# Kernel tuning notes

Hardware: AMD Instinct MI355X
Metric: run time of the kernel (lower is better)

Reference implementation:

```python
import jax, jax.numpy as jnp
import numpy as np

N, E, EL = 50000, 150000, 300000   # atoms, bonds(=line-graph nodes), line-graph edges
FN, FE, FX = 128, 128, 64          # atom, bond, angle feature dims (encode_dim)
H, D = 4, 64                        # num_heads, per-head hidden
SLOPE = 0.01                        # torch leaky_relu default


def _leaky(x):
    return jnp.where(x >= 0, x, SLOPE * x)


def _seg_softmax(logits, seg, n):
    # softmax over edges grouped by destination (DGL edge_softmax). logits [E, H]
    m = jax.ops.segment_max(logits, seg, num_segments=n)
    ex = jnp.exp(logits - m[seg])
    s = jax.ops.segment_sum(ex, seg, num_segments=n)
    return ex / s[seg]


def _seg_mean(x, seg, n):
    # mean of incoming edge feats per dst node; empty segments -> 0 (DGL behavior)
    s = jax.ops.segment_sum(x, seg, num_segments=n)
    c = jax.ops.segment_sum(jnp.ones((x.shape[0], 1), x.dtype), seg, num_segments=n)
    return s / jnp.maximum(c, 1.0)


def setup_inputs() -> dict:
    key = jax.random.key(0)
    ks = iter(jax.random.split(key, 40))
    nrm = lambda shape, sc=0.1: jax.random.normal(next(ks), shape, jnp.float32) * sc
    z = lambda n: jnp.zeros((n,), jnp.float32)
    inp = {
        'nfeats': nrm((N, FN), 1.0),
        'efeats': nrm((E, FE), 1.0),
        'xfeats': nrm((EL, FX), 1.0),
        # EGAT layer (atom graph)
        'e_Wni': nrm((H * D, FN)), 'e_Wnj': nrm((H * D, FN)), 'e_Wfij': nrm((H * D, FE)),
        'e_Wnode': nrm((H * D, FN + FE)), 'e_bnode': z(H * D),
        'e_attn': nrm((H, D)), 'e_bias': z(H * D),
        # Path_Complex line-graph branch
        'lg_Wni': nrm((H * D, D)), 'lg_Wnj': nrm((H * D, D)), 'lg_Wfij': nrm((H * D, FX)),
        'lg_Wnode': nrm((H * D, D + FX)), 'lg_bnode': z(H * D),
        'lg_attn': nrm((H, D)), 'lg_bias': z(H * D),
        # Path_Complex graph branch
        'g_Wni': nrm((H * D, D)), 'g_Wnj': nrm((H * D, D)), 'g_Wfij': nrm((H * D, D)),
        'g_Wnode': nrm((H * D, D + D)), 'g_bnode': z(H * D),
        'g_attn': nrm((H, D)), 'g_bias': z(H * D),
        # graph / line-graph connectivity
        'src': jax.random.randint(next(ks), (E,), 0, N, jnp.int32),
        'dst': jax.random.randint(next(ks), (E,), 0, N, jnp.int32),
        'lsrc': jax.random.randint(next(ks), (EL,), 0, E, jnp.int32),
        'ldst': jax.random.randint(next(ks), (EL,), 0, E, jnp.int32),
    }
    return inp


def _forward(nfeats, efeats, xfeats,
             e_Wni, e_Wnj, e_Wfij, e_Wnode, e_bnode, e_attn, e_bias,
             lg_Wni, lg_Wnj, lg_Wfij, lg_Wnode, lg_bnode, lg_attn, lg_bias,
             g_Wni, g_Wnj, g_Wfij, g_Wnode, g_bnode, g_attn, g_bias,
             src, dst, lsrc, ldst):
    # ---- EGAT layer on atom graph ----
    fo = _leaky((nfeats @ e_Wni.T)[src] + (nfeats @ e_Wnj.T)[dst] + efeats @ e_Wfij.T + e_bias)
    fov = fo.reshape(E, H, D)
    e_att = _seg_softmax((fov * e_attn[None]).sum(-1), dst, N)      # [E, H]
    agg = _seg_mean(efeats, dst, N)                                   # [N, FE]
    h = (jnp.concatenate([nfeats, agg], 1) @ e_Wnode.T + e_bnode).reshape(N, H, D)
    h_node = _leaky(jax.ops.segment_sum(h[src] * e_att[:, :, None], dst, num_segments=N)).sum(1)
    f_edge = fov.sum(1)                                               # [E, D]

    # ---- Path_Complex layer: line-graph (bond->angle) branch ----
    lgf = _leaky((f_edge @ lg_Wni.T)[lsrc] + (f_edge @ lg_Wnj.T)[ldst] + xfeats @ lg_Wfij.T + lg_bias)
    lgv = lgf.reshape(EL, H, D)
    a_lg = _seg_softmax((lgv * lg_attn[None]).sum(-1), ldst, E)      # [EL, H]
    aggx = _seg_mean(xfeats, ldst, E)                                 # [E, FX]
    m1 = (jnp.concatenate([f_edge, aggx], 1) @ lg_Wnode.T + lg_bnode).reshape(E, H, D)
    lg_h = _leaky(jax.ops.segment_sum(m1[lsrc] * a_lg[:, :, None], ldst, num_segments=E)).sum(1)

    # ---- Path_Complex layer: graph (atom->bond) branch ----
    gf = _leaky((h_node @ g_Wni.T)[src] + (h_node @ g_Wnj.T)[dst] + f_edge @ g_Wfij.T + g_bias)
    gv = gf.reshape(E, H, D)
    a_g = _seg_softmax((gv * g_attn[None]).sum(-1), dst, N)          # [E, H] -> l_graph ndata 'a'
    node_edge = h_node[src] + h_node[dst]
    m2 = (jnp.concatenate([node_edge, f_edge], 1) @ g_Wnode.T + g_bnode).reshape(E, H, D)
    # u_mul_v on line graph: message = h_out[lsrc] * a[ldst]
    g_h = _leaky(jax.ops.segment_sum(m2[lsrc] * a_g[ldst][:, :, None], ldst, num_segments=E)).sum(1)

    return g_h + lg_h                                                 # [E, D] updated bond feats


def reference(nfeats, efeats, xfeats,
              e_Wni, e_Wnj, e_Wfij, e_Wnode, e_bnode, e_attn, e_bias,
              lg_Wni, lg_Wnj, lg_Wfij, lg_Wnode, lg_bnode, lg_attn, lg_bias,
              g_Wni, g_Wnj, g_Wfij, g_Wnode, g_bnode, g_attn, g_bias,
              src, dst, lsrc, ldst):
    return _forward(nfeats, efeats, xfeats,
                    e_Wni, e_Wnj, e_Wfij, e_Wnode, e_bnode, e_attn, e_bias,
                    lg_Wni, lg_Wnj, lg_Wfij, lg_Wnode, lg_bnode, lg_attn, lg_bias,
                    g_Wni, g_Wnj, g_Wfij, g_Wnode, g_bnode, g_attn, g_bias,
                    src, dst, lsrc, ldst)
```

## Files before the change

### kernel.cpp

```cpp
#include <hip/hip_runtime.h>
#include <hip/hip_bf16.h>
#include <math.h>

typedef __hip_bfloat16 bf16;
typedef short bf16x8 __attribute__((ext_vector_type(8)));
typedef short s16x4 __attribute__((ext_vector_type(4)));
typedef float f32x4 __attribute__((ext_vector_type(4)));

__device__ __forceinline__ float b2f(bf16 x) { return __bfloat162float(x); }
__device__ __forceinline__ bf16  f2b(float x) { return __float2bfloat16(x); }
__device__ __forceinline__ float leaky(float x) { return x >= 0.0f ? x : 0.01f * x; }
__device__ __forceinline__ float sb2f(short s) {
  return __uint_as_float(((unsigned)(unsigned short)s) << 16);
}
__device__ __forceinline__ short f2bs(float x) {
  unsigned u = __float_as_uint(x);
  u += 0x7FFFu + ((u >> 16) & 1u);
  return (short)(u >> 16);
}
__device__ __forceinline__ float ldF(const void* p, size_t i, int f) {
  return f ? ((const float*)p)[i] : b2f(((const bf16*)p)[i]);
}
__device__ __forceinline__ bf16x8 ldA8(const char* row, int k, int f) {
  if (!f) return *(const bf16x8*)(row + (size_t)k * 2);
  const float4* p = (const float4*)(row + (size_t)k * 4);
  float4 a = p[0], b = p[1];
  bf16x8 r;
  r[0] = f2bs(a.x); r[1] = f2bs(a.y); r[2] = f2bs(a.z); r[3] = f2bs(a.w);
  r[4] = f2bs(b.x); r[5] = f2bs(b.y); r[6] = f2bs(b.z); r[7] = f2bs(b.w);
  return r;
}
__device__ __forceinline__ bf16x8 ldA8sum(const bf16* base, int K0, int s, int t, int k) {
  bf16x8 u = *(const bf16x8*)(base + (size_t)s * K0 + k);
  bf16x8 v = *(const bf16x8*)(base + (size_t)t * K0 + k);
  bf16x8 r;
#pragma unroll
  for (int j = 0; j < 8; ++j) r[j] = f2bs(sb2f(u[j]) + sb2f(v[j]));
  return r;
}

__global__ void k_detect(const unsigned* __restrict__ w, int* __restrict__ flag) {
  __shared__ int cnt[256];
  unsigned x = w[threadIdx.x];
  unsigned ex = (x >> 7) & 0xFFu;
  cnt[threadIdx.x] = (ex >= 96u && ex <= 144u) ? 1 : 0;
  __syncthreads();
  for (int s = 128; s > 0; s >>= 1) {
    if (threadIdx.x < s) cnt[threadIdx.x] += cnt[threadIdx.x + s];
    __syncthreads();
  }
  if (threadIdx.x == 0) *flag = (cnt[0] < 128) ? 1 : 0;
}

struct WArgs { const void* src[21]; int beg[22]; int len[21]; };
__global__ void k_cvt_all(WArgs wa, bf16* __restrict__ dst, int total,
                          const int* __restrict__ flagp) {
  int f = *flagp;
  for (int i = blockIdx.x * 256 + threadIdx.x; i < total; i += gridDim.x * 256) {
    int t = 0;
    while (t < 20 && i >= wa.beg[t + 1]) ++t;
    int loc = i - wa.beg[t];
    bf16 v = f2b(0.0f);
    if (loc < wa.len[t])
      v = f ? f2b(((const float*)wa.src[t])[loc]) : ((const bf16*)wa.src[t])[loc];
    dst[i] = v;
  }
}

__global__ void k_cvt3(const float* __restrict__ a, bf16* __restrict__ da, size_t na,
                       const float* __restrict__ b, bf16* __restrict__ db, size_t nb,
                       const float* __restrict__ c, bf16* __restrict__ dc, size_t nc,
                       const int* __restrict__ flagp) {
  if (!*flagp) return;
  size_t tot = (na + nb + nc) >> 2;
  for (size_t i = (size_t)blockIdx.x * 256 + threadIdx.x; i < tot;
       i += (size_t)gridDim.x * 256) {
    size_t j = i << 2;
    const float* s; bf16* d; size_t loc;
    if (j < na)           { s = a; d = da; loc = j; }
    else if (j < na + nb) { s = b; d = db; loc = j - na; }
    else                  { s = c; d = dc; loc = j - na - nb; }
    float4 v = *(const float4*)(s + loc);
    s16x4 o; o[0] = f2bs(v.x); o[1] = f2bs(v.y); o[2] = f2bs(v.z); o[3] = f2bs(v.w);
    *(s16x4*)(d + loc) = o;
  }
}

__global__ void k_izero(int* __restrict__ p, int n) {
  int i = blockIdx.x * 256 + threadIdx.x;
  for (; i < n; i += gridDim.x * 256) p[i] = 0;
}

__global__ void k_hist(const int* __restrict__ seg, int* __restrict__ deg, int n) {
  int i = blockIdx.x * 256 + threadIdx.x;
  if (i < n) atomicAdd(&deg[seg[i]], 1);
}

__global__ __launch_bounds__(256)
void k_scan_local(const int* __restrict__ deg, int* __restrict__ rp,
                  int* __restrict__ bsum, int n) {
  __shared__ int sh[256];
  int tid = threadIdx.x;
  int base = blockIdx.x * 4096 + tid * 16;
  int v[16]; int s = 0;
#pragma unroll
  for (int j = 0; j < 16; ++j) { v[j] = (base + j < n) ? deg[base + j] : 0; s += v[j]; }
  sh[tid] = s;
  __syncthreads();
  for (int o = 1; o < 256; o <<= 1) {
    int t = (tid >= o) ? sh[tid - o] : 0;
    __syncthreads();
    sh[tid] += t;
    __syncthreads();
  }
  int run = sh[tid] - s;
#pragma unroll
  for (int j = 0; j < 16; ++j) {
    run += v[j];
    if (base + j < n) rp[base + j + 1] = run;
  }
  if (tid == 255) bsum[blockIdx.x] = sh[255];
  if (blockIdx.x == 0 && tid == 0) rp[0] = 0;
}
__global__ __launch_bounds__(256)
void k_scan_bsum(int* __restrict__ bsum, int nb) {
  __shared__ int sh[256];
  __shared__ int carry;
  int tid = threadIdx.x;
  if (tid == 0) carry = 0;
  __syncthreads();
  for (int base = 0; base < nb; base += 256) {
    int i = base + tid;
    int v = (i < nb) ? bsum[i] : 0;
    sh[tid] = v;
    __syncthreads();
    for (int o = 1; o < 256; o <<= 1) {
      int t = (tid >= o) ? sh[tid - o] : 0;
      __syncthreads();
      sh[tid] += t;
      __syncthreads();
    }
    if (i < nb) bsum[i] = carry + sh[tid] - v;
    int tot = sh[255];
    __syncthreads();
    if (tid == 0) carry += tot;
    __syncthreads();
  }
}
__global__ __launch_bounds__(256)
void k_scan_add(int* __restrict__ rp, const int* __restrict__ bsum, int n) {
  int b = blockIdx.x + 1;
  int ofs = bsum[b];
  int base = b * 4096 + threadIdx.x * 16;
#pragma unroll
  for (int j = 0; j < 16; ++j) {
    int idx = base + j + 1;
    if (idx <= n) rp[idx] += ofs;
  }
}

__global__ void k_slot(const int* __restrict__ seg, const int* __restrict__ rp,
                       int* __restrict__ cur, int* __restrict__ eid,
                       const int* __restrict__ aux, int* __restrict__ auxval,
                       int* __restrict__ pos, int n) {
  int i = blockIdx.x * 256 + threadIdx.x;
  if (i >= n) return;
  int t = seg[i];
  int p = atomicAdd(&cur[t], 1);
  int j = rp[t] + p;
  eid[j] = i;
  if (auxval) auxval[j] = aux[i];
  if (pos) pos[i] = j;
}

__global__ void k_gmean(const void* __restrict__ X, const void* __restrict__ Xc, int mode,
                        const int* __restrict__ rp, const int* __restrict__ eid,
                        bf16* __restrict__ out, int n, int width,
                        const int* __restrict__ flagp) {
  int f = (mode == 2) ? *flagp : mode;
  if (Xc && f) { X = Xc; f = 0; }
  int d = threadIdx.x;
  int row = blockIdx.x * blockDim.y + threadIdx.y;
  if (row >= n) return;
  int b = rp[row], e = rp[row + 1];
  float s = 0.0f;
  for (int j = b; j < e; ++j) s += ldF(X, (size_t)eid[j] * width + d, f);
  out[(size_t)row * width + d] = f2b(s / fmaxf((float)(e - b), 1.0f));
}

__global__ __launch_bounds__(256)
void k_mgemm(const void* __restrict__ A0, const void* __restrict__ A0c, int m0mode, int K0,
             const void* __restrict__ A1, int m1mode, int Ktot,
             const bf16* __restrict__ W, int whs, const bf16* __restrict__ bias,
             bf16* __restrict__ C, int cs, int M,
             const int* __restrict__ gs, const int* __restrict__ gd,
             const int* __restrict__ flagp) {
  int tid = threadIdx.x;
  int w = tid >> 6, lane = tid & 63, l15 = lane & 15, q = lane >> 4;
  int h = blockIdx.y;
  int fl = *flagp;
  int f0 = (m0mode == 2) ? fl : m0mode;
  if (A0c && f0) { A0 = A0c; f0 = 0; }
  int f1 = (m1mode == 2) ? fl : m1mode;
  const bf16* Wh = W + (size_t)h * whs;
  int colofs = h * 64;
  int m0 = blockIdx.x * 64 + w * 16;
  int mA = m0 + l15; if (mA > M - 1) mA = M - 1;
  int sA = 0, tA = 0;
  const char* rowA0 = nullptr;
  if (gs) { sA = gs[mA]; tA = gd[mA]; }
  else rowA0 = (const char*)A0 + (size_t)mA * K0 * (f0 ? 4 : 2);
  const char* rowA1 = A1 ? (const char*)A1 + (size_t)mA * (Ktot - K0) * (f1 ? 4 : 2) : nullptr;

  f32x4 acc[4] = {{0,0,0,0},{0,0,0,0},{0,0,0,0},{0,0,0,0}};
  for (int k = q * 8; k < Ktot; k += 32) {
    bf16x8 a;
    if (k < K0) a = gs ? ldA8sum((const bf16*)A0, K0, sA, tA, k) : ldA8(rowA0, k, f0);
    else        a = ldA8(rowA1, k - K0, f1);
    const bf16* wb = Wh + (size_t)l15 * Ktot + k;
#pragma unroll
    for (int t = 0; t < 4; ++t)
      acc[t] = __builtin_amdgcn_mfma_f32_16x16x32_bf16(
          a, *(const bf16x8*)(wb + (size_t)(t * 16) * Ktot), acc[t], 0, 0, 0);
  }
#pragma unroll
  for (int t = 0; t < 4; ++t) {
    int col = t * 16 + l15;
    float bv = bias ? b2f(bias[colofs + col]) : 0.0f;
#pragma unroll
    for (int r = 0; r < 4; ++r) {
      int m = m0 + q * 4 + r;
      if (m < M) C[(size_t)m * cs + colofs + col] = f2b(acc[t][r] + bv);
    }
  }
}

__global__ __launch_bounds__(256)
void k_mgemm2(const void* __restrict__ A, const void* __restrict__ Ac, int mode, int K,
              const bf16* __restrict__ W1, const bf16* __restrict__ W2, int whs,
              bf16* __restrict__ C1, bf16* __restrict__ C2, int cs, int M,
              const int* __restrict__ flagp) {
  int tid = threadIdx.x;
  int w = tid >> 6, lane = tid & 63, l15 = lane & 15, q = lane >> 4;
  int h = blockIdx.y;
  int f = (mode == 2) ? *flagp : mode;
  if (Ac && f) { A = Ac; f = 0; }
  const bf16* W1h = W1 + (size_t)h * whs;
  const bf16* W2h = W2 + (size_t)h * whs;
  int colofs = h * 64;
  int m0 = blockIdx.x * 64 + w * 16;
  int mA = m0 + l15; if (mA > M - 1) mA = M - 1;
  const char* rowA = (const char*)A + (size_t)mA * K * (f ? 4 : 2);

  f32x4 a1[4] = {{0,0,0,0},{0,0,0,0},{0,0,0,0},{0,0,0,0}};
  f32x4 a2[4] = {{0,0,0,0},{0,0,0,0},{0,0,0,0},{0,0,0,0}};
  for (int k = q * 8; k < K; k += 32) {
    bf16x8 a = ldA8(rowA, k, f);
    const bf16* w1 = W1h + (size_t)l15 * K + k;
    const bf16* w2 = W2h + (size_t)l15 * K + k;
#pragma unroll
    for (int t = 0; t < 4; ++t) {
      a1[t] = __builtin_amdgcn_mfma_f32_16x16x32_bf16(
          a, *(const bf16x8*)(w1 + (size_t)(t * 16) * K), a1[t], 0, 0, 0);
      a2[t] = __builtin_amdgcn_mfma_f32_16x16x32_bf16(
          a, *(const bf16x8*)(w2 + (size_t)(t * 16) * K), a2[t], 0, 0, 0);
    }
  }
#pragma unroll
  for (int r = 0; r < 4; ++r) {
    int m = m0 + q * 4 + r;
    if (m < M) {
      s16x4 o1, o2;
#pragma unroll
      for (int t = 0; t < 4; ++t) { o1[t] = f2bs(a1[t][r]); o2[t] = f2bs(a2[t][r]); }
      *(s16x4*)(C1 + (size_t)m * cs + colofs + l15 * 4) = o1;
      *(s16x4*)(C2 + (size_t)m * cs + colofs + l15 * 4) = o2;
    }
  }
}

template<int NK>
__global__ __launch_bounds__(256)
void k_mcomb4(const void* __restrict__ A, const void* __restrict__ Ac, int mode,
              const bf16* __restrict__ W, int whs,
              const bf16* __restrict__ bias, const bf16* __restrict__ attn,
              const bf16* __restrict__ G1, const bf16* __restrict__ G2, int gstr,
              const int* __restrict__ gi, const int* __restrict__ gj,
              const int* __restrict__ posw,
              float* __restrict__ lg4, bf16* __restrict__ fout,
              int M, const int* __restrict__ flagp) {
  constexpr int K = NK * 32;
  int tid = threadIdx.x;
  int w = tid >> 6, lane = tid & 63, l15 = lane & 15, q = lane >> 4;
  int f = (mode == 2) ? *flagp : mode;
  if (Ac && f) { A = Ac; f = 0; }
  int m0 = blockIdx.x * 64 + w * 16;
  int mA = m0 + l15; if (mA > M - 1) mA = M - 1;
  const char* rowA = (const char*)A + (size_t)mA * K * (f ? 4 : 2);
  bf16x8 af[NK];
#pragma unroll
  for (int i = 0; i < NK; ++i) af[i] = ldA8(rowA, q * 8 + 32 * i, f);
  int sIdx[4], dIdx[4], pIdx[4]; bool okr[4];
#pragma unroll
  for (int r = 0; r < 4; ++r) {
    int m = m0 + q * 4 + r;
    okr[r] = m < M; int mc = okr[r] ? m : M - 1;
    sIdx[r] = gi[mc]; dIdx[r] = gj[mc];
    pIdx[r] = posw ? posw[mc] : mc;
  }
  s16x4 gv1[4][4], gv2[4][4];
#pragma unroll
  for (int r = 0; r < 4; ++r) {
    const s16x4* p1 = (const s16x4*)(G1 + (size_t)sIdx[r] * gstr) + l15;
    const s16x4* p2 = (const s16x4*)(G2 + (size_t)dIdx[r] * gstr) + l15;
#pragma unroll
    for (int h = 0; h < 4; ++h) { gv1[r][h] = p1[h * 16]; gv2[r][h] = p2[h * 16]; }
  }
  f32x4 fs[4] = {{0,0,0,0},{0,0,0,0},{0,0,0,0},{0,0,0,0}};
#pragma unroll
  for (int h = 0; h < 4; ++h) {
    const bf16* Wh = W + (size_t)h * whs;
    f32x4 acc[4] = {{0,0,0,0},{0,0,0,0},{0,0,0,0},{0,0,0,0}};
#pragma unroll
    for (int i = 0; i < NK; ++i) {
      const bf16* wb = Wh + (size_t)l15 * K + q * 8 + 32 * i;
#pragma unroll
      for (int t = 0; t < 4; ++t)
        acc[t] = __builtin_amdgcn_mfma_f32_16x16x32_bf16(
            af[i], *(const bf16x8*)(wb + (size_t)(t * 16) * K), acc[t], 0, 0, 0);
    }
    float bv[4], av[4];
#pragma unroll
    for (int t = 0; t < 4; ++t) {
      bv[t] = b2f(bias[h * 64 + t * 16 + l15]);
      av[t] = b2f(attn[h * 64 + t * 16 + l15]);
    }
    float part[4];
#pragma unroll
    for (int r = 0; r < 4; ++r) {
      float p = 0.0f;
#pragma unroll
      for (int t = 0; t < 4; ++t) {
        float v = acc[t][r] + bv[t] + sb2f(gv1[r][h][t]) + sb2f(gv2[r][h][t]);
        v = leaky(v);
        p += v * av[t];
        fs[t][r] += v;
      }
      part[r] = p;
    }
#pragma unroll
    for (int o = 1; o < 16; o <<= 1)
#pragma unroll
      for (int r = 0; r < 4; ++r) part[r] += __shfl_xor(part[r], o, 64);
    if (l15 == 0) {
#pragma unroll
      for (int r = 0; r < 4; ++r)
        if (okr[r]) lg4[(size_t)pIdx[r] * 4 + h] = part[r];
    }
  }
  if (fout) {
#pragma unroll
    for (int t = 0; t < 4; ++t) {
      int col = t * 16 + l15;
#pragma unroll
      for (int r = 0; r < 4; ++r)
        if (okr[r]) fout[(size_t)(m0 + q * 4 + r) * 64 + col] = f2b(fs[t][r]);
    }
  }
}

__global__ __launch_bounds__(256)
void k_mcomb(const void* __restrict__ A, const void* __restrict__ Ac, int mode, int K,
             const bf16* __restrict__ W, const bf16* __restrict__ bias,
             const bf16* __restrict__ attn,
             const bf16* __restrict__ G1, const bf16* __restrict__ G2, int gstr,
             const int* __restrict__ gi, const int* __restrict__ gj,
             const int* __restrict__ posw,
             float* __restrict__ lg, int M, const int* __restrict__ flagp) {
  int tid = threadIdx.x;
  int w = tid >> 6, lane = tid & 63, l15 = lane & 15, q = lane >> 4;
  int f = (mode == 2) ? *flagp : mode;
  if (Ac && f) { A = Ac; f = 0; }
  int m0 = blockIdx.x * 64 + w * 16;
  int mA = m0 + l15; if (mA > M - 1) mA = M - 1;
  const char* rowA = (const char*)A + (size_t)mA * K * (f ? 4 : 2);
  int mcs[4], pIdx[4]; bool okr[4];
#pragma unroll
  for (int r = 0; r < 4; ++r) {
    int m = m0 + q * 4 + r;
    okr[r] = m < M; mcs[r] = okr[r] ? m : M - 1;
    pIdx[r] = posw ? posw[mcs[r]] : mcs[r];
  }
  s16x4 gv1[4], gv2[4];
#pragma unroll
  for (int r = 0; r < 4; ++r) {
    gv1[r] = ((const s16x4*)(G1 + (size_t)gi[mcs[r]] * gstr))[l15];
    gv2[r] = ((const s16x4*)(G2 + (size_t)gj[mcs[r]] * gstr))[l15];
  }
  f32x4 acc[4] = {{0,0,0,0},{0,0,0,0},{0,0,0,0},{0,0,0,0}};
  for (int k = q * 8; k < K; k += 32) {
    bf16x8 a = ldA8(rowA, k, f);
    const bf16* wb = W + (size_t)l15 * K + k;
#pragma unroll
    for (int t = 0; t < 4; ++t)
      acc[t] = __builtin_amdgcn_mfma_f32_16x16x32_bf16(
          a, *(const bf16x8*)(wb + (size_t)(t * 16) * K), acc[t], 0, 0, 0);
  }
  float attv[4], bsv[4];
#pragma unroll
  for (int t = 0; t < 4; ++t) { attv[t] = b2f(attn[t*16+l15]); bsv[t] = b2f(bias[t*16+l15]); }
  float part[4];
#pragma unroll
  for (int r = 0; r < 4; ++r) {
    float p = 0.0f;
#pragma unroll
    for (int t = 0; t < 4; ++t) {
      float v = acc[t][r] + bsv[t] + sb2f(gv1[r][t]) + sb2f(gv2[r][t]);
      p += leaky(v) * attv[t];
    }
    part[r] = p;
  }
#pragma unroll
  for (int o = 1; o < 16; o <<= 1)
#pragma unroll
    for (int r = 0; r < 4; ++r) part[r] += __shfl_xor(part[r], o, 64);
  if (l15 == 0) {
#pragma unroll
    for (int r = 0; r < 4; ++r)
      if (okr[r]) lg[pIdx[r]] = part[r];
  }
}

__global__ __launch_bounds__(256)
void k_smax4_csr(float* __restrict__ lg, const int* __restrict__ rp, int n) {
  int tid = blockIdx.x * 256 + threadIdx.x;
  int row = tid >> 2, h = tid & 3;
  if (row >= n) return;
  int b = rp[row], e = rp[row + 1];
  float m = -INFINITY;
  for (int j = b; j < e; ++j) m = fmaxf(m, lg[(size_t)j * 4 + h]);
  float s = 0.0f;
  for (int j = b; j < e; ++j) {
    float ex = expf(lg[(size_t)j * 4 + h] - m);
    lg[(size_t)j * 4 + h] = ex;
    s += ex;
  }
  float inv = 1.0f / s;
  for (int j = b; j < e; ++j) lg[(size_t)j * 4 + h] *= inv;
}
__global__ __launch_bounds__(256)
void k_smax4_eid(float* __restrict__ lg, const int* __restrict__ rp,
                 const int* __restrict__ eid, int n) {
  int tid = blockIdx.x * 256 + threadIdx.x;
  int row = tid >> 2, h = tid & 3;
  if (row >= n) return;
  int b = rp[row], e = rp[row + 1];
  float m = -INFINITY;
  for (int j = b; j < e; ++j) m = fmaxf(m, lg[(size_t)eid[j] * 4 + h]);
  float s = 0.0f;
  for (int j = b; j < e; ++j) {
    float ex = expf(lg[(size_t)eid[j] * 4 + h] - m);
    lg[(size_t)eid[j] * 4 + h] = ex;
    s += ex;
  }
  float inv = 1.0f / s;
  for (int j = b; j < e; ++j) lg[(size_t)eid[j] * 4 + h] *= inv;
}
__global__ __launch_bounds__(256)
void k_smax1_csr(float* __restrict__ lg, const int* __restrict__ rp, int n) {
  int row = blockIdx.x * 256 + threadIdx.x;
  if (row >= n) return;
  int b = rp[row], e = rp[row + 1];
  float m = -INFINITY;
  for (int j = b; j < e; ++j) m = fmaxf(m, lg[j]);
  float s = 0.0f;
  for (int j = b; j < e; ++j) { float ex = expf(lg[j] - m); lg[j] = ex; s += ex; }
  float inv = 1.0f / s;
  for (int j = b; j < e; ++j) lg[j] *= inv;
}

__global__ __launch_bounds__(256)
void k_ghnode(const bf16* __restrict__ H, const float* __restrict__ lg4c,
              const int* __restrict__ rp, const int* __restrict__ srcv,
              bf16* __restrict__ hnode, int N) {
  int d = threadIdx.x, h = threadIdx.y;
  int n = blockIdx.x;
  int b = rp[n], e = rp[n + 1];
  float s = 0.0f;
  for (int j = b; j < e; ++j)
    s += b2f(H[(size_t)srcv[j] * 256 + h * 64 + d]) * lg4c[(size_t)j * 4 + h];
  float v = leaky(s);
  __shared__ float sh[4][64];
  if (h > 0) sh[h][d] = v;
  __syncthreads();
  if (h == 0)
    hnode[(size_t)n * 64 + d] = f2b(v + sh[1][d] + sh[2][d] + sh[3][d]);
}

__global__ void k_gout2(const bf16* __restrict__ M1, const float* __restrict__ lgE,
                        const int* __restrict__ rp, const int* __restrict__ lsv,
                        float* __restrict__ out, int E, int first) {
  int d = threadIdx.x;
  int t = blockIdx.x * 4 + threadIdx.y;
  if (t >= E) return;
  int b = rp[t], e = rp[t + 1];
  float s = 0.0f;
  for (int j = b; j < e; ++j)
    s += b2f(M1[(size_t)lsv[j] * 64 + d]) * lgE[j];
  float val = leaky(s);
  if (first) out[(size_t)t * 64 + d] = val;
  else       out[(size_t)t * 64 + d] += val;
}

__global__ void k_gout3(const bf16* __restrict__ M2, const float* __restrict__ lg4n,
                        const int* __restrict__ rp, const int* __restrict__ lsv,
                        float* __restrict__ out, int E, int h) {
  int d = threadIdx.x;
  int t = blockIdx.x * 4 + threadIdx.y;
  if (t >= E) return;
  int b = rp[t], e = rp[t + 1];
  float s = 0.0f;
  for (int j = b; j < e; ++j) s += b2f(M2[(size_t)lsv[j] * 64 + d]);
  float a = lg4n[(size_t)t * 4 + h];
  out[(size_t)t * 64 + d] += leaky(a * s);
}

__global__ void k_addpair(const bf16* __restrict__ hn, const int* __restrict__ src,
                          const int* __restrict__ dst, bf16* __restrict__ ne, int E) {
  int d = threadIdx.x;
  int e = blockIdx.x * 4 + threadIdx.y;
  if (e >= E) return;
  ne[(size_t)e * 64 + d] =
      f2b(b2f(hn[(size_t)src[e] * 64 + d]) + b2f(hn[(size_t)dst[e] * 64 + d]));
}

__global__ void k_cast(void* __restrict__ out, const float* __restrict__ a, size_t n,
                       const int* __restrict__ flagp) {
  int f = *flagp;
  size_t i = (size_t)blockIdx.x * blockDim.x + threadIdx.x;
  size_t st = (size_t)gridDim.x * blockDim.x;
  for (; i < n; i += st) {
    if (f) ((float*)out)[i] = a[i];
    else   ((bf16*)out)[i] = f2b(a[i]);
  }
}

extern "C" void kernel_launch(void* const* d_in, const int* in_sizes, int n_in,
                              void* d_out, int out_size, void* d_ws, size_t ws_size,
                              hipStream_t stream) {
  const int* src  = (const int*)d_in[24];
  const int* dst  = (const int*)d_in[25];
  const int* lsrc = (const int*)d_in[26];
  const int* ldst = (const int*)d_in[27];

  const int N  = in_sizes[0] / 128;
  const int E  = in_sizes[24];
  const int EL = in_sizes[26];
  (void)n_in; (void)out_size; (void)ws_size;

  char* base = (char*)d_ws;
  size_t off = 0;
  auto alloc = [&](size_t bytes) -> char* {
    char* p = base + off;
    off = (off + bytes + 255) & ~(size_t)255;
    return p;
  };
  int* flag = (int*)alloc(256);
  size_t wofs[28]; size_t wtot = 0;
  for (int i = 3; i <= 23; ++i) { wofs[i] = wtot; wtot += (size_t)((in_sizes[i] + 127) & ~127); }
  bf16* WA = (bf16*)alloc(wtot * 2);

  int*   tmpi  = (int*)alloc((size_t)2 * E * 4);
  int*   rpN   = (int*)alloc((size_t)(N + 1) * 4);
  int*   eidN  = (int*)alloc((size_t)E * 4);
  int*   srcv  = (int*)alloc((size_t)E * 4);
  int*   posN  = (int*)alloc((size_t)E * 4);
  int*   rpE   = (int*)alloc((size_t)(E + 1) * 4);
  int*   eidEL = (int*)alloc((size_t)EL * 4);
  int*   lsv   = (int*)alloc((size_t)EL * 4);
  int*   posE  = (int*)alloc((size_t)EL * 4);
  int*   bsum  = (int*)alloc(((size_t)((E > N ? E : N) + 4095) / 4096 + 8) * 4);
  bf16*  fedge = (bf16*)alloc((size_t)E * 64 * 2);
  bf16*  hnode = (bf16*)alloc((size_t)N * 64 * 2);
  float* outacc= (float*)alloc((size_t)E * 64 * 4);
  bf16*  aggB  = (bf16*)alloc((size_t)E * 64 * 2);
  bf16*  SA    = (bf16*)alloc((size_t)N * 256 * 2 > (size_t)E * 64 * 2
                              ? (size_t)N * 256 * 2 : (size_t)E * 64 * 2);
  bf16*  SB    = (bf16*)alloc((size_t)N * 256 * 2 > (size_t)E * 64 * 2
                              ? (size_t)N * 256 * 2 : (size_t)E * 64 * 2);
  float* logE4 = (float*)alloc((size_t)E * 4 * 4);
  float* logh  = (float*)alloc((size_t)EL * 4);
  bf16*  nb    = (bf16*)alloc((size_t)N * 128 * 2);

  bf16* eb = (bf16*)outacc;
  bf16* xb = (bf16*)d_out;

  dim3 blk(256);
  const unsigned tN = (N + 63) / 64, tEg = (E + 63) / 64, tELg = (EL + 63) / 64;
  const unsigned gE4 = (E + 3) / 4, gN4 = (N + 3) / 4;
  const unsigned cE = (E + 255) / 256, cEL = (EL + 255) / 256;
  const int nbN = (N + 4095) / 4096, nbE = (E + 4095) / 4096;

  k_detect<<<dim3(1), blk, 0, stream>>>((const unsigned*)d_in[0], flag);
  WArgs wa;
  for (int i = 3; i <= 23; ++i) {
    wa.src[i - 3] = d_in[i];
    wa.beg[i - 3] = (int)wofs[i];
    wa.len[i - 3] = in_sizes[i];
  }
  wa.beg[21] = (int)wtot;
  k_cvt_all<<<dim3(512), blk, 0, stream>>>(wa, WA, (int)wtot, flag);
  k_cvt3<<<dim3(2048), blk, 0, stream>>>(
      (const float*)d_in[0], nb, (size_t)N * 128,
      (const float*)d_in[1], eb, (size_t)E * 128,
      (const float*)d_in[2], xb, (size_t)EL * 64, flag);

  int* deg = tmpi; int* cur = tmpi + E;
  k_izero<<<dim3(1024), blk, 0, stream>>>(tmpi, 2 * E);
  k_hist<<<dim3(cE), blk, 0, stream>>>(dst, deg, E);
  k_scan_local<<<dim3(nbN), blk, 0, stream>>>(deg, rpN, bsum, N);
  k_scan_bsum<<<dim3(1), blk, 0, stream>>>(bsum, nbN);
  if (nbN > 1) k_scan_add<<<dim3(nbN - 1), blk, 0, stream>>>(rpN, bsum, N);
  k_slot<<<dim3(cE), blk, 0, stream>>>(dst, rpN, cur, eidN, src, srcv, posN, E);
  k_izero<<<dim3(1024), blk, 0, stream>>>(tmpi, 2 * E);
  k_hist<<<dim3(cEL), blk, 0, stream>>>(ldst, deg, EL);
  k_scan_local<<<dim3(nbE), blk, 0, stream>>>(deg, rpE, bsum, E);
  k_scan_bsum<<<dim3(1), blk, 0, stream>>>(bsum, nbE);
  if (nbE > 1) k_scan_add<<<dim3(nbE - 1), blk, 0, stream>>>(rpE, bsum, E);
  k_slot<<<dim3(cEL), blk, 0, stream>>>(ldst, rpE, cur, eidEL, lsrc, lsv, posE, EL);

  k_gmean<<<dim3((N + 1) / 2), dim3(128, 2), 0, stream>>>(d_in[1], eb, 2, rpN, eidN,
                                                          aggB, N, 128, flag);
  k_mgemm2<<<dim3(tN, 4), blk, 0, stream>>>(d_in[0], nb, 2, 128, WA + wofs[3], WA + wofs[4],
                                            8192, SA, SB, 256, N, flag);
  k_mcomb4<4><<<dim3(tEg), blk, 0, stream>>>(d_in[1], eb, 2, WA + wofs[5], 8192,
      WA + wofs[9], WA + wofs[8], SA, SB, 256, src, dst, posN, logE4, fedge, E, flag);
  k_smax4_csr<<<dim3((N * 4 + 255) / 256), blk, 0, stream>>>(logE4, rpN, N);
  k_mgemm<<<dim3(tN, 4), blk, 0, stream>>>(d_in[0], nb, 2, 128, aggB, 0, 256,
      WA + wofs[6], 16384, WA + wofs[7], SA, 256, N, nullptr, nullptr, flag);
  k_ghnode<<<dim3(N), dim3(64, 4), 0, stream>>>(SA, logE4, rpN, srcv, hnode, N);

  k_gmean<<<dim3(gE4), dim3(64, 4), 0, stream>>>(d_in[2], xb, 2, rpE, eidEL, aggB, E, 64, flag);
  for (int h = 0; h < 4; ++h) {
    k_mgemm2<<<dim3(tEg), blk, 0, stream>>>(fedge, nullptr, 0, 64,
        WA + wofs[10] + h * 4096, WA + wofs[11] + h * 4096, 0, SA, SB, 64, E, flag);
    k_mcomb<<<dim3(tELg), blk, 0, stream>>>(d_in[2], xb, 2, 64,
        WA + wofs[12] + h * 4096, WA + wofs[16] + h * 64, WA + wofs[15] + h * 64,
        SA, SB, 64, lsrc, ldst, posE, logh, EL, flag);
    k_smax1_csr<<<dim3((E + 255) / 256), blk, 0, stream>>>(logh, rpE, E);
    k_mgemm<<<dim3(tEg, 1), blk, 0, stream>>>(fedge, nullptr, 0, 64, aggB, 0, 128,
        WA + wofs[13] + (size_t)h * 8192, 0, WA + wofs[14] + h * 64,
        SA, 64, E, nullptr, nullptr, flag);
    k_gout2<<<dim3(gE4), dim3(64, 4), 0, stream>>>(SA, logh, rpE, lsv,
                                                   outacc, E, h == 0 ? 1 : 0);
  }

  k_mgemm2<<<dim3(tN, 4), blk, 0, stream>>>(hnode, nullptr, 0, 64, WA + wofs[17], WA + wofs[18],
                                            4096, SA, SB, 256, N, flag);
  k_mcomb4<2><<<dim3(tEg), blk, 0, stream>>>(fedge, nullptr, 0, WA + wofs[19], 4096,
      WA + wofs[23], WA + wofs[22], SA, SB, 256, src, dst, nullptr, logE4, nullptr, E, flag);
  k_smax4_eid<<<dim3((N * 4 + 255) / 256), blk, 0, stream>>>(logE4, rpN, eidN, N);
  k_addpair<<<dim3(gE4), dim3(64, 4), 0, stream>>>(hnode, src, dst, aggB, E);
  for (int h = 0; h < 4; ++h) {
    k_mgemm<<<dim3(tEg, 1), blk, 0, stream>>>(aggB, nullptr, 0, 64, fedge, 0, 128,
        WA + wofs[20] + (size_t)h * 8192, 0, WA + wofs[21] + h * 64,
        SB, 64, E, nullptr, nullptr, flag);
    k_gout3<<<dim3(gE4), dim3(64, 4), 0, stream>>>(SB, logE4, rpE, lsv,
                                                   outacc, E, h);
  }

  k_cast<<<dim3(2048), blk, 0, stream>>>(d_out, outacc, (size_t)E * 64, flag);
}
```

Measured before the change: 1.804 ms.

## Permute bond data into dst-sorted CSR order and translate indices accordingly

Bond features and all bond-indexed intermediates (fedge, logE4, aggregated messages) are now stored in dst-sorted CSR order. A gather kernel builds the permuted bf16 copy, and line-graph indices are remapped through posN. This lets the atom-level mean and softmax read contiguous rows instead of going through eid indirection, and it removes the separate eid-based softmax kernel. In exchange it adds a permutation pass, an index translation kernel and extra index arrays, and the final outputs must be mapped back through posN lookups.

```diff
diff --git a/kernel.cpp b/kernel.cpp
--- a/kernel.cpp
+++ b/kernel.cpp
@@ -67,22 +67,38 @@
   }
 }
 
-__global__ void k_cvt3(const float* __restrict__ a, bf16* __restrict__ da, size_t na,
-                       const float* __restrict__ b, bf16* __restrict__ db, size_t nb,
+__global__ void k_cvt2(const float* __restrict__ a, bf16* __restrict__ da, size_t na,
                        const float* __restrict__ c, bf16* __restrict__ dc, size_t nc,
                        const int* __restrict__ flagp) {
   if (!*flagp) return;
-  size_t tot = (na + nb + nc) >> 2;
+  size_t tot = (na + nc) >> 2;
   for (size_t i = (size_t)blockIdx.x * 256 + threadIdx.x; i < tot;
        i += (size_t)gridDim.x * 256) {
     size_t j = i << 2;
     const float* s; bf16* d; size_t loc;
-    if (j < na)           { s = a; d = da; loc = j; }
-    else if (j < na + nb) { s = b; d = db; loc = j - na; }
-    else                  { s = c; d = dc; loc = j - na - nb; }
+    if (j < na) { s = a; d = da; loc = j; }
+    else        { s = c; d = dc; loc = j - na; }
     float4 v = *(const float4*)(s + loc);
     s16x4 o; o[0] = f2bs(v.x); o[1] = f2bs(v.y); o[2] = f2bs(v.z); o[3] = f2bs(v.w);
     *(s16x4*)(d + loc) = o;
+  }
+}
+
+__global__ void k_cvtp(const void* __restrict__ X, const int* __restrict__ eid,
+                       bf16* __restrict__ out, int n, const int* __restrict__ flagp) {
+  int f = *flagp;
+  int row = blockIdx.x * 4 + threadIdx.y;
+  if (row >= n) return;
+  int e = eid[row];
+  int d0 = threadIdx.x * 2;
+  if (f) {
+    float2 v = *(const float2*)((const float*)X + (size_t)e * 128 + d0);
+    unsigned pack = ((unsigned)(unsigned short)f2bs(v.y) << 16) |
+                    (unsigned)(unsigned short)f2bs(v.x);
+    *(unsigned*)((char*)out + (size_t)row * 256 + d0 * 2) = pack;
+  } else {
+    *(unsigned*)((char*)out + (size_t)row * 256 + d0 * 2) =
+        *(const unsigned*)((const char*)X + (size_t)e * 256 + d0 * 2);
   }
 }
 
@@ -161,7 +177,8 @@
 
 __global__ void k_slot(const int* __restrict__ seg, const int* __restrict__ rp,
                        int* __restrict__ cur, int* __restrict__ eid,
-                       const int* __restrict__ aux, int* __restrict__ auxval,
+                       const int* __restrict__ aux1, int* __restrict__ av1,
+                       const int* __restrict__ aux2, int* __restrict__ av2,
                        int* __restrict__ pos, int n) {
   int i = blockIdx.x * 256 + threadIdx.x;
   if (i >= n) return;
@@ -169,12 +186,25 @@
   int p = atomicAdd(&cur[t], 1);
   int j = rp[t] + p;
   eid[j] = i;
-  if (auxval) auxval[j] = aux[i];
+  if (av1) av1[j] = aux1[i];
+  if (av2) av2[j] = aux2[i];
   if (pos) pos[i] = j;
+}
+
+__global__ void k_xlat(const int* __restrict__ lsrc, const int* __restrict__ ldst,
+                       const int* __restrict__ posN,
+                       int* __restrict__ lsvE, int* __restrict__ ldvE,
+                       int* __restrict__ lsvC, int n) {
+  int i = blockIdx.x * 256 + threadIdx.x;
+  if (i >= n) return;
+  lsvE[i] = posN[lsrc[i]];
+  ldvE[i] = posN[ldst[i]];
+  lsvC[i] = posN[lsvC[i]];
 }
 
 __global__ void k_gmean(const void* __restrict__ X, const void* __restrict__ Xc, int mode,
                         const int* __restrict__ rp, const int* __restrict__ eid,
+                        const int* __restrict__ orow,
                         bf16* __restrict__ out, int n, int width,
                         const int* __restrict__ flagp) {
   int f = (mode == 2) ? *flagp : mode;
@@ -184,8 +214,10 @@
   if (row >= n) return;
   int b = rp[row], e = rp[row + 1];
   float s = 0.0f;
-  for (int j = b; j < e; ++j) s += ldF(X, (size_t)eid[j] * width + d, f);
-  out[(size_t)row * width + d] = f2b(s / fmaxf((float)(e - b), 1.0f));
+  for (int j = b; j < e; ++j)
+    s += ldF(X, (size_t)(eid ? eid[j] : j) * width + d, f);
+  int orw = orow ? orow[row] : row;
+  out[(size_t)orw * width + d] = f2b(s / fmaxf((float)(e - b), 1.0f));
 }
 
 __global__ __launch_bounds__(256)
@@ -193,7 +225,6 @@
              const void* __restrict__ A1, int m1mode, int Ktot,
              const bf16* __restrict__ W, int whs, const bf16* __restrict__ bias,
              bf16* __restrict__ C, int cs, int M,
-             const int* __restrict__ gs, const int* __restrict__ gd,
              const int* __restrict__ flagp) {
   int tid = threadIdx.x;
   int w = tid >> 6, lane = tid & 63, l15 = lane & 15, q = lane >> 4;
@@ -206,16 +237,13 @@
   int colofs = h * 64;
   int m0 = blockIdx.x * 64 + w * 16;
   int mA = m0 + l15; if (mA > M - 1) mA = M - 1;
-  int sA = 0, tA = 0;
-  const char* rowA0 = nullptr;
-  if (gs) { sA = gs[mA]; tA = gd[mA]; }
-  else rowA0 = (const char*)A0 + (size_t)mA * K0 * (f0 ? 4 : 2);
+  const char* rowA0 = (const char*)A0 + (size_t)mA * K0 * (f0 ? 4 : 2);
   const char* rowA1 = A1 ? (const char*)A1 + (size_t)mA * (Ktot - K0) * (f1 ? 4 : 2) : nullptr;
 
   f32x4 acc[4] = {{0,0,0,0},{0,0,0,0},{0,0,0,0},{0,0,0,0}};
   for (int k = q * 8; k < Ktot; k += 32) {
     bf16x8 a;
-    if (k < K0) a = gs ? ldA8sum((const bf16*)A0, K0, sA, tA, k) : ldA8(rowA0, k, f0);
+    if (k < K0) a = ldA8(rowA0, k, f0);
     else        a = ldA8(rowA1, k - K0, f1);
     const bf16* wb = Wh + (size_t)l15 * Ktot + k;
 #pragma unroll
@@ -281,32 +309,28 @@
 
 template<int NK>
 __global__ __launch_bounds__(256)
-void k_mcomb4(const void* __restrict__ A, const void* __restrict__ Ac, int mode,
-              const bf16* __restrict__ W, int whs,
-              const bf16* __restrict__ bias, const bf16* __restrict__ attn,
-              const bf16* __restrict__ G1, const bf16* __restrict__ G2, int gstr,
-              const int* __restrict__ gi, const int* __restrict__ gj,
-              const int* __restrict__ posw,
-              float* __restrict__ lg4, bf16* __restrict__ fout,
-              int M, const int* __restrict__ flagp) {
+void k_mcomb4C(const bf16* __restrict__ A,
+               const bf16* __restrict__ W, int whs,
+               const bf16* __restrict__ bias, const bf16* __restrict__ attn,
+               const bf16* __restrict__ G1, const bf16* __restrict__ G2, int gstr,
+               const int* __restrict__ sv, const int* __restrict__ dv,
+               float* __restrict__ lg4, bf16* __restrict__ fout, int M) {
   constexpr int K = NK * 32;
   int tid = threadIdx.x;
   int w = tid >> 6, lane = tid & 63, l15 = lane & 15, q = lane >> 4;
-  int f = (mode == 2) ? *flagp : mode;
-  if (Ac && f) { A = Ac; f = 0; }
   int m0 = blockIdx.x * 64 + w * 16;
   int mA = m0 + l15; if (mA > M - 1) mA = M - 1;
-  const char* rowA = (const char*)A + (size_t)mA * K * (f ? 4 : 2);
+  const bf16* rowA = A + (size_t)mA * K;
   bf16x8 af[NK];
 #pragma unroll
-  for (int i = 0; i < NK; ++i) af[i] = ldA8(rowA, q * 8 + 32 * i, f);
-  int sIdx[4], dIdx[4], pIdx[4]; bool okr[4];
+  for (int i = 0; i < NK; ++i) af[i] = *(const bf16x8*)(rowA + q * 8 + 32 * i);
+  int sIdx[4], dIdx[4], mcs[4]; bool okr[4];
 #pragma unroll
   for (int r = 0; r < 4; ++r) {
     int m = m0 + q * 4 + r;
     okr[r] = m < M; int mc = okr[r] ? m : M - 1;
-    sIdx[r] = gi[mc]; dIdx[r] = gj[mc];
-    pIdx[r] = posw ? posw[mc] : mc;
+    mcs[r] = mc;
+    sIdx[r] = sv[mc]; dIdx[r] = dv[mc];
   }
   s16x4 gv1[4][4], gv2[4][4];
 #pragma unroll
@@ -355,7 +379,7 @@
     if (l15 == 0) {
 #pragma unroll
       for (int r = 0; r < 4; ++r)
-        if (okr[r]) lg4[(size_t)pIdx[r] * 4 + h] = part[r];
+        if (okr[r]) lg4[(size_t)mcs[r] * 4 + h] = part[r];
     }
   }
   if (fout) {
@@ -449,24 +473,6 @@
   for (int j = b; j < e; ++j) lg[(size_t)j * 4 + h] *= inv;
 }
 __global__ __launch_bounds__(256)
-void k_smax4_eid(float* __restrict__ lg, const int* __restrict__ rp,
-                 const int* __restrict__ eid, int n) {
-  int tid = blockIdx.x * 256 + threadIdx.x;
-  int row = tid >> 2, h = tid & 3;
-  if (row >= n) return;
-  int b = rp[row], e = rp[row + 1];
-  float m = -INFINITY;
-  for (int j = b; j < e; ++j) m = fmaxf(m, lg[(size_t)eid[j] * 4 + h]);
-  float s = 0.0f;
-  for (int j = b; j < e; ++j) {
-    float ex = expf(lg[(size_t)eid[j] * 4 + h] - m);
-    lg[(size_t)eid[j] * 4 + h] = ex;
-    s += ex;
-  }
-  float inv = 1.0f / s;
-  for (int j = b; j < e; ++j) lg[(size_t)eid[j] * 4 + h] *= inv;
-}
-__global__ __launch_bounds__(256)
 void k_smax1_csr(float* __restrict__ lg, const int* __restrict__ rp, int n) {
   int row = blockIdx.x * 256 + threadIdx.x;
   if (row >= n) return;
@@ -513,6 +519,7 @@
 }
 
 __global__ void k_gout3(const bf16* __restrict__ M2, const float* __restrict__ lg4n,
+                        const int* __restrict__ posN,
                         const int* __restrict__ rp, const int* __restrict__ lsv,
                         float* __restrict__ out, int E, int h) {
   int d = threadIdx.x;
@@ -521,17 +528,17 @@
   int b = rp[t], e = rp[t + 1];
   float s = 0.0f;
   for (int j = b; j < e; ++j) s += b2f(M2[(size_t)lsv[j] * 64 + d]);
-  float a = lg4n[(size_t)t * 4 + h];
+  float a = lg4n[(size_t)posN[t] * 4 + h];
   out[(size_t)t * 64 + d] += leaky(a * s);
 }
 
-__global__ void k_addpair(const bf16* __restrict__ hn, const int* __restrict__ src,
-                          const int* __restrict__ dst, bf16* __restrict__ ne, int E) {
+__global__ void k_addpairC(const bf16* __restrict__ hn, const int* __restrict__ sv,
+                           const int* __restrict__ dv, bf16* __restrict__ ne, int E) {
   int d = threadIdx.x;
-  int e = blockIdx.x * 4 + threadIdx.y;
-  if (e >= E) return;
-  ne[(size_t)e * 64 + d] =
-      f2b(b2f(hn[(size_t)src[e] * 64 + d]) + b2f(hn[(size_t)dst[e] * 64 + d]));
+  int j = blockIdx.x * 4 + threadIdx.y;
+  if (j >= E) return;
+  ne[(size_t)j * 64 + d] =
+      f2b(b2f(hn[(size_t)sv[j] * 64 + d]) + b2f(hn[(size_t)dv[j] * 64 + d]));
 }
 
 __global__ void k_cast(void* __restrict__ out, const float* __restrict__ a, size_t n,
@@ -574,10 +581,13 @@
   int*   rpN   = (int*)alloc((size_t)(N + 1) * 4);
   int*   eidN  = (int*)alloc((size_t)E * 4);
   int*   srcv  = (int*)alloc((size_t)E * 4);
+  int*   dstv  = (int*)alloc((size_t)E * 4);
   int*   posN  = (int*)alloc((size_t)E * 4);
   int*   rpE   = (int*)alloc((size_t)(E + 1) * 4);
   int*   eidEL = (int*)alloc((size_t)EL * 4);
   int*   lsv   = (int*)alloc((size_t)EL * 4);
+  int*   lsvE  = (int*)alloc((size_t)EL * 4);
+  int*   ldvE  = (int*)alloc((size_t)EL * 4);
   int*   posE  = (int*)alloc((size_t)EL * 4);
   int*   bsum  = (int*)alloc(((size_t)((E > N ? E : N) + 4095) / 4096 + 8) * 4);
   bf16*  fedge = (bf16*)alloc((size_t)E * 64 * 2);
@@ -592,12 +602,12 @@
   float* logh  = (float*)alloc((size_t)EL * 4);
   bf16*  nb    = (bf16*)alloc((size_t)N * 128 * 2);
 
-  bf16* eb = (bf16*)outacc;
-  bf16* xb = (bf16*)d_out;
+  bf16* ebC = (bf16*)outacc;
+  bf16* xb  = (bf16*)d_out;
 
   dim3 blk(256);
   const unsigned tN = (N + 63) / 64, tEg = (E + 63) / 64, tELg = (EL + 63) / 64;
-  const unsigned gE4 = (E + 3) / 4, gN4 = (N + 3) / 4;
+  const unsigned gE4 = (E + 3) / 4;
   const unsigned cE = (E + 255) / 256, cEL = (EL + 255) / 256;
   const int nbN = (N + 4095) / 4096, nbE = (E + 4095) / 4096;
 
@@ -610,9 +620,8 @@
   }
   wa.beg[21] = (int)wtot;
   k_cvt_all<<<dim3(512), blk, 0, stream>>>(wa, WA, (int)wtot, flag);
-  k_cvt3<<<dim3(2048), blk, 0, stream>>>(
+  k_cvt2<<<dim3(2048), blk, 0, stream>>>(
       (const float*)d_in[0], nb, (size_t)N * 128,
-      (const float*)d_in[1], eb, (size_t)E * 128,
       (const float*)d_in[2], xb, (size_t)EL * 64, flag);
 
   int* deg = tmpi; int* cur = tmpi + E;
@@ -621,51 +630,55 @@
   k_scan_local<<<dim3(nbN), blk, 0, stream>>>(deg, rpN, bsum, N);
   k_scan_bsum<<<dim3(1), blk, 0, stream>>>(bsum, nbN);
   if (nbN > 1) k_scan_add<<<dim3(nbN - 1), blk, 0, stream>>>(rpN, bsum, N);
-  k_slot<<<dim3(cE), blk, 0, stream>>>(dst, rpN, cur, eidN, src, srcv, posN, E);
+  k_slot<<<dim3(cE), blk, 0, stream>>>(dst, rpN, cur, eidN, src, srcv, dst, dstv, posN, E);
+  k_cvtp<<<dim3(gE4), dim3(64, 4), 0, stream>>>(d_in[1], eidN, ebC, E, flag);
   k_izero<<<dim3(1024), blk, 0, stream>>>(tmpi, 2 * E);
   k_hist<<<dim3(cEL), blk, 0, stream>>>(ldst, deg, EL);
   k_scan_local<<<dim3(nbE), blk, 0, stream>>>(deg, rpE, bsum, E);
   k_scan_bsum<<<dim3(1), blk, 0, stream>>>(bsum, nbE);
   if (nbE > 1) k_scan_add<<<dim3(nbE - 1), blk, 0, stream>>>(rpE, bsum, E);
-  k_slot<<<dim3(cEL), blk, 0, stream>>>(ldst, rpE, cur, eidEL, lsrc, lsv, posE, EL);
-
-  k_gmean<<<dim3((N + 1) / 2), dim3(128, 2), 0, stream>>>(d_in[1], eb, 2, rpN, eidN,
-                                                          aggB, N, 128, flag);
+  k_slot<<<dim3(cEL), blk, 0, stream>>>(ldst, rpE, cur, eidEL, lsrc, lsv, nullptr, nullptr,
+                                        posE, EL);
+  k_xlat<<<dim3(cEL), blk, 0, stream>>>(lsrc, ldst, posN, lsvE, ldvE, lsv, EL);
+
+  k_gmean<<<dim3((N + 1) / 2), dim3(128, 2), 0, stream>>>(ebC, nullptr, 0, rpN, nullptr,
+                                                          nullptr, aggB, N, 128, flag);
   k_mgemm2<<<dim3(tN, 4), blk, 0, stream>>>(d_in[0], nb, 2, 128, WA + wofs[3], WA + wofs[4],
                                             8192, SA, SB, 256, N, flag);
-  k_mcomb4<4><<<dim3(tEg), blk, 0, stream>>>(d_in[1], eb, 2, WA + wofs[5], 8192,
-      WA + wofs[9], WA + wofs[8], SA, SB, 256, src, dst, posN, logE4, fedge, E, flag);
+  k_mcomb4C<4><<<dim3(tEg), blk, 0, stream>>>(ebC, WA + wofs[5], 8192,
+      WA + wofs[9], WA + wofs[8], SA, SB, 256, srcv, dstv, logE4, fedge, E);
   k_smax4_csr<<<dim3((N * 4 + 255) / 256), blk, 0, stream>>>(logE4, rpN, N);
   k_mgemm<<<dim3(tN, 4), blk, 0, stream>>>(d_in[0], nb, 2, 128, aggB, 0, 256,
-      WA + wofs[6], 16384, WA + wofs[7], SA, 256, N, nullptr, nullptr, flag);
+      WA + wofs[6], 16384, WA + wofs[7], SA, 256, N, flag);
   k_ghnode<<<dim3(N), dim3(64, 4), 0, stream>>>(SA, logE4, rpN, srcv, hnode, N);
 
-  k_gmean<<<dim3(gE4), dim3(64, 4), 0, stream>>>(d_in[2], xb, 2, rpE, eidEL, aggB, E, 64, flag);
+  k_gmean<<<dim3(gE4), dim3(64, 4), 0, stream>>>(d_in[2], xb, 2, rpE, eidEL, posN,
+                                                 aggB, E, 64, flag);
   for (int h = 0; h < 4; ++h) {
     k_mgemm2<<<dim3(tEg), blk, 0, stream>>>(fedge, nullptr, 0, 64,
         WA + wofs[10] + h * 4096, WA + wofs[11] + h * 4096, 0, SA, SB, 64, E, flag);
     k_mcomb<<<dim3(tELg), blk, 0, stream>>>(d_in[2], xb, 2, 64,
         WA + wofs[12] + h * 4096, WA + wofs[16] + h * 64, WA + wofs[15] + h * 64,
-        SA, SB, 64, lsrc, ldst, posE, logh, EL, flag);
+        SA, SB, 64, lsvE, ldvE, posE, logh, EL, flag);
     k_smax1_csr<<<dim3((E + 255) / 256), blk, 0, stream>>>(logh, rpE, E);
     k_mgemm<<<dim3(tEg, 1), blk, 0, stream>>>(fedge, nullptr, 0, 64, aggB, 0, 128,
         WA + wofs[13] + (size_t)h * 8192, 0, WA + wofs[14] + h * 64,
-        SA, 64, E, nullptr, nullptr, flag);
+        SA, 64, E, flag);
     k_gout2<<<dim3(gE4), dim3(64, 4), 0, stream>>>(SA, logh, rpE, lsv,
                                                    outacc, E, h == 0 ? 1 : 0);
   }
 
-  k_mgemm2<<<dim3(tN, 4), blk, 0, stream>>>(hnode, nullptr, 0, 64, WA + wofs[17], WA + wofs[18],
-                                            4096, SA, SB, 256, N, flag);
-  k_mcomb4<2><<<dim3(tEg), blk, 0, stream>>>(fedge, nullptr, 0, WA + wofs[19], 4096,
-      WA + wofs[23], WA + wofs[22], SA, SB, 256, src, dst, nullptr, logE4, nullptr, E, flag);
-  k_smax4_eid<<<dim3((N * 4 + 255) / 256), blk, 0, stream>>>(logE4, rpN, eidN, N);
-  k_addpair<<<dim3(gE4), dim3(64, 4), 0, stream>>>(hnode, src, dst, aggB, E);
+  k_mgemm2<<<dim3(tN, 4), blk, 0, stream>>>(hnode, nullptr, 0, 64, WA + wofs[17],
+                                            WA + wofs[18], 4096, SA, SB, 256, N, flag);
+  k_mcomb4C<2><<<dim3(tEg), blk, 0, stream>>>(fedge, WA + wofs[19], 4096,
+      WA + wofs[23], WA + wofs[22], SA, SB, 256, srcv, dstv, logE4, nullptr, E);
+  k_smax4_csr<<<dim3((N * 4 + 255) / 256), blk, 0, stream>>>(logE4, rpN, N);
+  k_addpairC<<<dim3(gE4), dim3(64, 4), 0, stream>>>(hnode, srcv, dstv, aggB, E);
   for (int h = 0; h < 4; ++h) {
     k_mgemm<<<dim3(tEg, 1), blk, 0, stream>>>(aggB, nullptr, 0, 64, fedge, 0, 128,
         WA + wofs[20] + (size_t)h * 8192, 0, WA + wofs[21] + h * 64,
-        SB, 64, E, nullptr, nullptr, flag);
-    k_gout3<<<dim3(gE4), dim3(64, 4), 0, stream>>>(SB, logE4, rpE, lsv,
+        SA, 64, E, flag);
+    k_gout3<<<dim3(gE4), dim3(64, 4), 0, stream>>>(SA, logE4, posN, rpE, lsv,
                                                    outacc, E, h);
   }
 
```

Result: slower. 1.862 ms (+3.2%).
